# Kernel tuning notes

Measured on AMD Instinct MI355X. Metric: run time of the kernel, lower is better.

## Reference

```python
import jax, jax.numpy as jnp
import numpy as np

T, D, E = 65536, 1024, 64  # tokens, d_model, n_experts

def setup_inputs() -> dict:
    key = jax.random.key(0)
    k1, k2 = jax.random.split(key)
    x = jax.random.normal(k1, (T, D), dtype=jnp.float32)
    Wg = jax.random.normal(k2, (D, E), dtype=jnp.float32) * (1.0 / np.sqrt(D))
    return {"x": x, "Wg": Wg, "top_k": 2}

def reference(x, Wg, top_k):
    # Token-to-expert gating: logits -> softmax -> top-k -> renormalized combine weights.
    logits = jnp.einsum('td,de->te', x, Wg)            # [T, E]
    probs = jax.nn.softmax(logits, axis=-1)            # [T, E]
    topk_vals, topk_idx = jax.lax.top_k(probs, top_k)  # [T, k], [T, k]
    combine = topk_vals / jnp.sum(topk_vals, axis=-1, keepdims=True)  # renormalize over selected experts
    return combine, topk_idx, probs
```

## Files before the change

### kernel.cpp

```cpp
#include <hip/hip_runtime.h>
#include <hip/hip_bf16.h>
#include <math.h>


#define D_DIM 1024
#define E_DIM 64
#define TM    64
#define BK    32
#define NCH   (D_DIM / BK)
#define TPB   256
#define MARGIN 1e-3f
#define WT_U4  16384

typedef float f32x4 __attribute__((ext_vector_type(4)));
typedef short s16x8 __attribute__((ext_vector_type(8)));

__device__ __forceinline__ ushort bf16u(float f) {
  union { __hip_bfloat16 b; ushort u; } cv;
  cv.b = __float2bfloat16(f);
  return cv.u;
}

__device__ __forceinline__ void async_cp16(void* l, const void* g) {
  __builtin_amdgcn_global_load_lds(
      (const __attribute__((address_space(1))) void*)g,
      (__attribute__((address_space(3))) void*)l, 16, 0, 0);
}

__global__ void wprep_kernel(const float* __restrict__ Wg, uint4* __restrict__ w4,
                             unsigned* __restrict__ ctr) {
  const int gi = blockIdx.x * blockDim.x + threadIdx.x;
  if (gi == 0) ctr[0] = 0u;
  const int p    = gi >> 13;
  const int ch   = (gi >> 8) & 31;
  const int e    = (gi >> 2) & 63;
  const int slot = gi & 3;
  const int g    = slot ^ ((e >> 1) & 3);
  const int k0   = ch * BK + g * 8;
  unsigned pk[4];
#pragma unroll
  for (int jj = 0; jj < 4; ++jj) {
    const float w0 = Wg[(k0 + 2 * jj    ) * E_DIM + e];
    const float w1 = Wg[(k0 + 2 * jj + 1) * E_DIM + e];
    if (p == 0) {
      pk[jj] = ((unsigned)bf16u(w1) << 16) | (unsigned)bf16u(w0);
    } else {
      const float l0 = w0 - __uint_as_float((unsigned)bf16u(w0) << 16);
      const float l1 = w1 - __uint_as_float((unsigned)bf16u(w1) << 16);
      pk[jj] = ((unsigned)bf16u(l1) << 16) | (unsigned)bf16u(l0);
    }
  }
  w4[gi] = make_uint4(pk[0], pk[1], pk[2], pk[3]);
}

struct Frag2 { s16x8 hi, lo; };

__device__ __forceinline__ Frag2 cvt8(const float4 a, const float4 b) {
  const float f[8] = {a.x, a.y, a.z, a.w, b.x, b.y, b.z, b.w};
  Frag2 r;
#pragma unroll
  for (int i = 0; i < 8; ++i) {
    const ushort h = bf16u(f[i]);
    r.hi[i] = (short)h;
    const float lf = f[i] - __uint_as_float((unsigned)h << 16);
    r.lo[i] = (short)bf16u(lf);
  }
  return r;
}

__global__ __launch_bounds__(TPB, 4) void router_mfma(
    const float* __restrict__ x, const uint4* __restrict__ wt,
    float* __restrict__ out, unsigned* __restrict__ ctr,
    unsigned* __restrict__ list, int rcap, int T)
{
  __shared__ uint4 sx[2][512];
  __shared__ uint4 sw[2][512];

  const int tid  = threadIdx.x;
  const int wid  = tid >> 6;
  const int lane = tid & 63;
  const int c    = lane & 15;
  const int q    = lane >> 4;
  const int trow = wid * 16 + c;
  const int tok  = blockIdx.x * TM + trow;
  const size_t xbase = (size_t)blockIdx.x * TM * D_DIM;

  f32x4 acc[4];
#pragma unroll
  for (int et = 0; et < 4; ++et) acc[et] = (f32x4){0.f, 0.f, 0.f, 0.f};

  const int j0 = wid * 2;

  auto stage = [&](int ch, int buf) {
#pragma unroll
    for (int i = 0; i < 2; ++i) {
      const int j    = j0 + i;
      const int rowr = j * 8 + (lane >> 3);
      const float* src = x + xbase + (size_t)rowr * D_DIM + ch * BK
                       + (((lane & 7) ^ (lane >> 3)) << 2);
      async_cp16(&sx[buf][j * 64], src);
    }
#pragma unroll
    for (int i = 0; i < 2; ++i) {
      const int j = j0 + i;
      const int G = j * 64 + lane;
      const int p = G >> 8, r = G & 255;
      const uint4* src = wt + (size_t)(p * 32 + ch) * 256 + r;
      async_cp16(&sw[buf][j * 64], src);
    }
  };

  stage(0, 0);
  __syncthreads();

  for (int ch = 0; ch < NCH; ++ch) {
    const int cur = ch & 1;
    if (ch + 1 < NCH) stage(ch + 1, cur ^ 1);

    const float4* xb4 = (const float4*)&sx[cur][0];
    const int rb = trow * 8, key = c & 7;
    const float4 x0 = xb4[rb + ((2 * q + 0) ^ key)];
    const float4 x1 = xb4[rb + ((2 * q + 1) ^ key)];
    const Frag2 b = cvt8(x0, x1);

    const s16x8* wb = (const s16x8*)&sw[cur][0];
    const int slotr = q ^ ((c >> 1) & 3);
    s16x8 ah[4], al[4];
#pragma unroll
    for (int et = 0; et < 4; ++et) {
      const int e = et * 16 + c;
      ah[et] = wb[e * 4 + slotr];
      al[et] = wb[256 + e * 4 + slotr];
    }
#pragma unroll
    for (int et = 0; et < 4; ++et) {
      f32x4 a = acc[et];
      a = __builtin_amdgcn_mfma_f32_16x16x32_bf16(ah[et], b.hi, a, 0, 0, 0);
      a = __builtin_amdgcn_mfma_f32_16x16x32_bf16(ah[et], b.lo, a, 0, 0, 0);
      acc[et] = a;
    }
#pragma unroll
    for (int et = 0; et < 4; ++et)
      acc[et] = __builtin_amdgcn_mfma_f32_16x16x32_bf16(al[et], b.hi, acc[et], 0, 0, 0);

    __syncthreads();
  }

  const size_t Ts = (size_t)T;
  float* const comb = out;
  float* const idxo = out + 2 * Ts;
  float* const prob = out + 4 * Ts;

  float v[16];
#pragma unroll
  for (int et = 0; et < 4; ++et)
#pragma unroll
    for (int r = 0; r < 4; ++r) v[et * 4 + r] = acc[et][r];

  float v1 = v[0], v2 = -INFINITY, v3 = -INFINITY;
  int   i1 = q * 4, i2 = 0;
#pragma unroll
  for (int et = 0; et < 4; ++et)
#pragma unroll
    for (int r = 0; r < 4; ++r) {
      if (et == 0 && r == 0) continue;
      const float p  = v[et * 4 + r];
      const int   ei = et * 16 + q * 4 + r;
      if (p > v1)      { v3 = v2; v2 = v1; i2 = i1; v1 = p; i1 = ei; }
      else if (p > v2) { v3 = v2; v2 = p;  i2 = ei; }
      else if (p > v3) { v3 = p; }
    }
#pragma unroll
  for (int d = 16; d <= 32; d <<= 1) {
    const float ov1 = __shfl_xor(v1, d); const int oi1 = __shfl_xor(i1, d);
    const float ov2 = __shfl_xor(v2, d); const int oi2 = __shfl_xor(i2, d);
    const float ov3 = __shfl_xor(v3, d);
    const bool  ob1 = (ov1 > v1) || (ov1 == v1 && oi1 < i1);
    const float w1v = ob1 ? ov1 : v1;  const int w1i = ob1 ? oi1 : i1;
    const float l1v = ob1 ? v1  : ov1; const int l1i = ob1 ? i1  : oi1;
    const float w2v = ob1 ? ov2 : v2;  const int w2i = ob1 ? oi2 : i2;
    const float ls2 = ob1 ? v2  : ov2;
    const float ws3 = ob1 ? ov3 : v3;
    const bool  b2  = (l1v > w2v) || (l1v == w2v && l1i < w2i);
    const float a2v = b2 ? l1v : w2v; const int a2i = b2 ? l1i : w2i;
    const float a3v = b2 ? fmaxf(w2v, ls2) : fmaxf(l1v, ws3);
    v1 = w1v; i1 = w1i; v2 = a2v; i2 = a2i; v3 = a3v;
  }

  float s = 0.f;
#pragma unroll
  for (int i = 0; i < 16; ++i) { v[i] = __expf(v[i] - v1); s += v[i]; }
  s += __shfl_xor(s, 16);
  s += __shfl_xor(s, 32);
  const float inv = 1.f / s;

#pragma unroll
  for (int et = 0; et < 4; ++et)
    *(float4*)&prob[(size_t)tok * E_DIM + et * 16 + q * 4] =
        make_float4(v[et * 4 + 0] * inv, v[et * 4 + 1] * inv,
                    v[et * 4 + 2] * inv, v[et * 4 + 3] * inv);

  if (q == 0) {
    if ((v1 - v2 < MARGIN) || (v2 - v3 < MARGIN)) {
      const unsigned slot = atomicAdd(ctr, 1u);
      if ((int)slot < rcap) list[slot] = (unsigned)tok;
    }
    const float c1 = 1.f / (1.f + __expf(v2 - v1));
    *(float2*)&comb[2 * (size_t)tok] = make_float2(c1, 1.f - c1);
    *(float2*)&idxo[2 * (size_t)tok] = make_float2((float)i1, (float)i2);
  }
}

__global__ __launch_bounds__(256) void repair_kernel(
    const float* __restrict__ x, const float* __restrict__ Wg,
    float* __restrict__ out, const unsigned* __restrict__ ctr,
    const unsigned* __restrict__ list, int rcap, int T)
{
  __shared__ double part[4][E_DIM];
  const int tid = threadIdx.x;
  const int e   = tid & 63;
  const int s   = tid >> 6;
  const unsigned total = ctr[0];
  const unsigned n = total < (unsigned)rcap ? total : (unsigned)rcap;

  for (unsigned j = blockIdx.x; j < n; j += gridDim.x) {
    const int t = (int)list[j];
    const float* xr = x  + (size_t)t * D_DIM + s * 256;
    const float* wr = Wg + (size_t)(s * 256) * E_DIM + e;
    double a = 0.0;
#pragma unroll 8
    for (int d = 0; d < 256; ++d)
      a += (double)xr[d] * (double)wr[(size_t)d * E_DIM];
    part[s][e] = a;
    __syncthreads();
    if (tid < 64) {
      const float l = (float)(part[0][e] + part[1][e] + part[2][e] + part[3][e]);
      float m = l;
#pragma unroll
      for (int d2 = 1; d2 < 64; d2 <<= 1) m = fmaxf(m, __shfl_xor(m, d2));
      const float p = expf(l - m);
      float ss = p;
#pragma unroll
      for (int d2 = 1; d2 < 64; d2 <<= 1) ss += __shfl_xor(ss, d2);
      out[4 * (size_t)T + (size_t)t * E_DIM + e] = p / ss;
      float v1 = l, v2 = -INFINITY; int i1 = e, i2 = 0;
#pragma unroll
      for (int d2 = 1; d2 < 64; d2 <<= 1) {
        const float ov1 = __shfl_xor(v1, d2); const int oi1 = __shfl_xor(i1, d2);
        const float ov2 = __shfl_xor(v2, d2); const int oi2 = __shfl_xor(i2, d2);
        const bool  ob1 = (ov1 > v1) || (ov1 == v1 && oi1 < i1);
        const float w1v = ob1 ? ov1 : v1;  const int w1i = ob1 ? oi1 : i1;
        const float l1v = ob1 ? v1  : ov1; const int l1i = ob1 ? i1  : oi1;
        const float w2v = ob1 ? ov2 : v2;  const int w2i = ob1 ? oi2 : i2;
        const bool  b2  = (l1v > w2v) || (l1v == w2v && l1i < w2i);
        v1 = w1v; i1 = w1i;
        v2 = b2 ? l1v : w2v; i2 = b2 ? l1i : w2i;
      }
      if (e == 0) {
        const float c1 = 1.f / (1.f + expf(v2 - v1));
        out[2 * (size_t)t]     = c1;
        out[2 * (size_t)t + 1] = 1.f - c1;
        out[2 * (size_t)T + 2 * (size_t)t]     = (float)i1;
        out[2 * (size_t)T + 2 * (size_t)t + 1] = (float)i2;
      }
    }
    __syncthreads();
  }
}

extern "C" void kernel_launch(void* const* d_in, const int* in_sizes, int n_in,
                              void* d_out, int out_size, void* d_ws, size_t ws_size,
                              hipStream_t stream) {
  const float* x  = (const float*)d_in[0];
  const float* Wg = (const float*)d_in[1];
  float* out = (float*)d_out;
  uint4* wt  = (uint4*)d_ws;
  unsigned* ctr  = (unsigned*)d_ws + WT_U4 * 4;
  unsigned* list = ctr + 1;
  const int T = in_sizes[0] / D_DIM;

  long avail = ((long)ws_size - (long)(WT_U4 * 16 + 4)) / 4;
  int rcap = avail < 0 ? 0 : (avail > 8192 ? 8192 : (int)avail);

  wprep_kernel<<<dim3(WT_U4 / TPB), dim3(TPB), 0, stream>>>(Wg, wt, ctr);
  router_mfma<<<dim3(T / TM), dim3(TPB), 0, stream>>>(x, wt, out, ctr, list, rcap, T);
  repair_kernel<<<dim3(1024), dim3(256), 0, stream>>>(x, Wg, out, ctr, list, rcap, T);
}
```

Measured before the change: 411.1 us.

## Load x directly into registers and stage only weights through LDS

The router GEMM no longer copies x through shared memory. Each thread now loads its token's x slices straight from global memory into registers, double-buffered across two register sets. Only the split-bf16 weights are staged asynchronously through LDS, in larger 128-wide K chunks. Blocks grow to 512 threads and 128 tokens, which halves the number of barriers and shares each weight tile across more tokens, at the cost of more registers per thread and possibly less coalesced x loads. The epilogue and any LDS it uses under the new TPB/TM may not match, so correctness is uncertain.

Result: faster. 392.0 us (-4.7%).

```diff
diff --git a/kernel.cpp b/kernel.cpp
--- a/kernel.cpp
+++ b/kernel.cpp
@@ -5,10 +5,10 @@
 
 #define D_DIM 1024
 #define E_DIM 64
-#define TM    64
-#define BK    32
-#define NCH   (D_DIM / BK)
-#define TPB   256
+#define TM    128
+#define BK    128
+#define NCHB  (D_DIM / BK)
+#define TPB   512
 #define MARGIN 1e-3f
 #define WT_U4  16384
 
@@ -36,7 +36,7 @@
   const int e    = (gi >> 2) & 63;
   const int slot = gi & 3;
   const int g    = slot ^ ((e >> 1) & 3);
-  const int k0   = ch * BK + g * 8;
+  const int k0   = ch * 32 + g * 8;
   unsigned pk[4];
 #pragma unroll
   for (int jj = 0; jj < 4; ++jj) {
@@ -73,76 +73,78 @@
     float* __restrict__ out, unsigned* __restrict__ ctr,
     unsigned* __restrict__ list, int rcap, int T)
 {
-  __shared__ uint4 sx[2][512];
-  __shared__ uint4 sw[2][512];
+  __shared__ uint4 swW[2][2048];
 
   const int tid  = threadIdx.x;
   const int wid  = tid >> 6;
   const int lane = tid & 63;
   const int c    = lane & 15;
   const int q    = lane >> 4;
-  const int trow = wid * 16 + c;
-  const int tok  = blockIdx.x * TM + trow;
-  const size_t xbase = (size_t)blockIdx.x * TM * D_DIM;
+  const int tok  = blockIdx.x * TM + wid * 16 + c;
 
   f32x4 acc[4];
 #pragma unroll
   for (int et = 0; et < 4; ++et) acc[et] = (f32x4){0.f, 0.f, 0.f, 0.f};
 
-  const int j0 = wid * 2;
-
-  auto stage = [&](int ch, int buf) {
-#pragma unroll
-    for (int i = 0; i < 2; ++i) {
-      const int j    = j0 + i;
-      const int rowr = j * 8 + (lane >> 3);
-      const float* src = x + xbase + (size_t)rowr * D_DIM + ch * BK
-                       + (((lane & 7) ^ (lane >> 3)) << 2);
-      async_cp16(&sx[buf][j * 64], src);
-    }
-#pragma unroll
-    for (int i = 0; i < 2; ++i) {
-      const int j = j0 + i;
-      const int G = j * 64 + lane;
-      const int p = G >> 8, r = G & 255;
-      const uint4* src = wt + (size_t)(p * 32 + ch) * 256 + r;
-      async_cp16(&sw[buf][j * 64], src);
-    }
+  const float* __restrict__ xb = x + (size_t)tok * D_DIM + q * 8;
+
+  const int pw = wid >> 2;
+  const int rr = (wid & 3) * 64 + lane;
+
+  auto stageW = [&](int ch, int buf) {
+#pragma unroll
+    for (int r = 0; r < 4; ++r)
+      async_cp16(&swW[buf][r * 512 + wid * 64],
+                 wt + (size_t)(pw * 32 + ch * 4 + r) * 256 + rr);
   };
 
-  stage(0, 0);
+  auto loadx = [&](float4 (&xr)[8], int ch) {
+#pragma unroll
+    for (int sub = 0; sub < 4; ++sub)
+#pragma unroll
+      for (int h = 0; h < 2; ++h)
+        xr[sub * 2 + h] = *(const float4*)(xb + ch * BK + sub * 32 + h * 4);
+  };
+
+  const int slotr = q ^ ((c >> 1) & 3);
+
+  auto compute = [&](const float4 (&xr)[8], int buf) {
+#pragma unroll
+    for (int sub = 0; sub < 4; ++sub) {
+      const Frag2 b = cvt8(xr[sub * 2], xr[sub * 2 + 1]);
+      const s16x8* wb = (const s16x8*)&swW[buf][sub * 512];
+      s16x8 ah[4], al[4];
+#pragma unroll
+      for (int et = 0; et < 4; ++et) {
+        const int e = et * 16 + c;
+        ah[et] = wb[e * 4 + slotr];
+        al[et] = wb[256 + e * 4 + slotr];
+      }
+#pragma unroll
+      for (int et = 0; et < 4; ++et) {
+        f32x4 a = acc[et];
+        a = __builtin_amdgcn_mfma_f32_16x16x32_bf16(ah[et], b.hi, a, 0, 0, 0);
+        a = __builtin_amdgcn_mfma_f32_16x16x32_bf16(ah[et], b.lo, a, 0, 0, 0);
+        acc[et] = a;
+      }
+#pragma unroll
+      for (int et = 0; et < 4; ++et)
+        acc[et] = __builtin_amdgcn_mfma_f32_16x16x32_bf16(al[et], b.hi, acc[et], 0, 0, 0);
+    }
+  };
+
+  float4 xA[8], xB[8];
+
+  stageW(0, 0);
+  loadx(xA, 0);
   __syncthreads();
 
-  for (int ch = 0; ch < NCH; ++ch) {
-    const int cur = ch & 1;
-    if (ch + 1 < NCH) stage(ch + 1, cur ^ 1);
-
-    const float4* xb4 = (const float4*)&sx[cur][0];
-    const int rb = trow * 8, key = c & 7;
-    const float4 x0 = xb4[rb + ((2 * q + 0) ^ key)];
-    const float4 x1 = xb4[rb + ((2 * q + 1) ^ key)];
-    const Frag2 b = cvt8(x0, x1);
-
-    const s16x8* wb = (const s16x8*)&sw[cur][0];
-    const int slotr = q ^ ((c >> 1) & 3);
-    s16x8 ah[4], al[4];
-#pragma unroll
-    for (int et = 0; et < 4; ++et) {
-      const int e = et * 16 + c;
-      ah[et] = wb[e * 4 + slotr];
-      al[et] = wb[256 + e * 4 + slotr];
-    }
-#pragma unroll
-    for (int et = 0; et < 4; ++et) {
-      f32x4 a = acc[et];
-      a = __builtin_amdgcn_mfma_f32_16x16x32_bf16(ah[et], b.hi, a, 0, 0, 0);
-      a = __builtin_amdgcn_mfma_f32_16x16x32_bf16(ah[et], b.lo, a, 0, 0, 0);
-      acc[et] = a;
-    }
-#pragma unroll
-    for (int et = 0; et < 4; ++et)
-      acc[et] = __builtin_amdgcn_mfma_f32_16x16x32_bf16(al[et], b.hi, acc[et], 0, 0, 0);
-
+  for (int cp = 0; cp < NCHB; cp += 2) {
+    if (cp + 1 < NCHB) { stageW(cp + 1, 1); loadx(xB, cp + 1); }
+    compute(xA, 0);
+    __syncthreads();
+    if (cp + 2 < NCHB) { stageW(cp + 2, 0); loadx(xA, cp + 2); }
+    compute(xB, 1);
     __syncthreads();
   }
 
@@ -282,7 +284,7 @@
   long avail = ((long)ws_size - (long)(WT_U4 * 16 + 4)) / 4;
   int rcap = avail < 0 ? 0 : (avail > 8192 ? 8192 : (int)avail);
 
-  wprep_kernel<<<dim3(WT_U4 / TPB), dim3(TPB), 0, stream>>>(Wg, wt, ctr);
+  wprep_kernel<<<dim3(WT_U4 / 256), dim3(256), 0, stream>>>(Wg, wt, ctr);
   router_mfma<<<dim3(T / TM), dim3(TPB), 0, stream>>>(x, wt, out, ctr, list, rcap, T);
   repair_kernel<<<dim3(1024), dim3(256), 0, stream>>>(x, Wg, out, ctr, list, rcap, T);
 }
```
